# Kernel tuning notes

Hardware: AMD Instinct MI355X
Metric: run time of the kernel (lower is better)

The kernel has to match this reference:

```python
import jax, jax.numpy as jnp
import numpy as np

DIM = 256
H = W = 56
WS = 7           # window size
SHIFT = 3        # shift size
NH = 8           # num heads
HD = DIM // NH   # head dim
N = WS * WS      # tokens per window
SCALE = HD ** -0.5
EPS = 1e-5


def _rel_pos_index():
    coords = np.stack(np.meshgrid(np.arange(WS), np.arange(WS), indexing='ij'))  # (2,WS,WS)
    cf = coords.reshape(2, -1)                                # (2, N)
    rel = cf[:, :, None] - cf[:, None, :]                     # (2, N, N)
    rel = rel.transpose(1, 2, 0).astype(np.int64)             # (N, N, 2)
    rel[:, :, 0] += WS - 1
    rel[:, :, 1] += WS - 1
    rel[:, :, 0] *= 2 * WS - 1
    return rel.sum(-1)                                        # (N, N)

REL_IDX = _rel_pos_index()


def _attn_mask():
    # standard Swin shift mask: (nW, N, N) with 0 / -100
    img = np.zeros((H, W))
    cnt = 0
    for hs in (slice(0, -WS), slice(-WS, -SHIFT), slice(-SHIFT, None)):
        for ws in (slice(0, -WS), slice(-WS, -SHIFT), slice(-SHIFT, None)):
            img[hs, ws] = cnt
            cnt += 1
    win = img.reshape(H // WS, WS, W // WS, WS).transpose(0, 2, 1, 3).reshape(-1, N)  # (nW, N)
    diff = win[:, None, :] - win[:, :, None]
    return np.where(diff != 0, -100.0, 0.0).astype(np.float32)

ATTN_MASK = jnp.asarray(_attn_mask())  # (nW, N, N)


def _ln(x, g, b):
    mu = jnp.mean(x, -1, keepdims=True)
    var = jnp.mean(jnp.square(x - mu), -1, keepdims=True)
    return (x - mu) * jax.lax.rsqrt(var + EPS) * g + b


def _win_part(x):
    # (B,H,W,C) -> (B*nW, N, C)
    B, _, _, C = x.shape
    x = x.reshape(B, H // WS, WS, W // WS, WS, C)
    return x.transpose(0, 1, 3, 2, 4, 5).reshape(-1, N, C)


def _win_rev(xw, B):
    # (B*nW, N, C) -> (B,H,W,C)
    C = xw.shape[-1]
    x = xw.reshape(B, H // WS, W // WS, WS, WS, C)
    return x.transpose(0, 1, 3, 2, 4, 5).reshape(B, H, W, C)


def setup_inputs() -> dict:
    key = jax.random.key(0)
    ks = jax.random.split(key, 6)
    return {
        'x': jax.random.normal(ks[0], (32, H * W, DIM), jnp.float32),
        'norm1_g': jnp.ones((DIM,), jnp.float32),
        'norm1_b': jnp.zeros((DIM,), jnp.float32),
        'qkv_w': jax.random.normal(ks[1], (3 * DIM, DIM), jnp.float32) * 0.02,
        'qkv_b': jnp.zeros((3 * DIM,), jnp.float32),
        'rel_table': jax.random.normal(ks[2], ((2 * WS - 1) ** 2, NH), jnp.float32) * 0.02,
        'proj_w': jax.random.normal(ks[3], (DIM, DIM), jnp.float32) * 0.02,
        'proj_b': jnp.zeros((DIM,), jnp.float32),
        'norm2_g': jnp.ones((DIM,), jnp.float32),
        'norm2_b': jnp.zeros((DIM,), jnp.float32),
        'fc1_w': jax.random.normal(ks[4], (4 * DIM, DIM), jnp.float32) * 0.02,
        'fc1_b': jnp.zeros((4 * DIM,), jnp.float32),
        'fc2_w': jax.random.normal(ks[5], (DIM, 4 * DIM), jnp.float32) * 0.02,
        'fc2_b': jnp.zeros((DIM,), jnp.float32),
    }


def reference(x, norm1_g, norm1_b, qkv_w, qkv_b, rel_table, proj_w, proj_b,
              norm2_g, norm2_b, fc1_w, fc1_b, fc2_w, fc2_b):
    B = x.shape[0]
    shortcut = x
    h = _ln(x, norm1_g, norm1_b).reshape(B, H, W, DIM)
    # cyclic shift
    h = jnp.roll(h, (-SHIFT, -SHIFT), axis=(1, 2))
    xw = _win_part(h)                                  # (B*nW, N, C)
    Bw = xw.shape[0]
    qkv = (xw @ qkv_w.T + qkv_b).reshape(Bw, N, 3, NH, HD).transpose(2, 0, 3, 1, 4)
    q, k, v = qkv[0] * SCALE, qkv[1], qkv[2]           # (Bw, NH, N, HD)
    attn = jnp.einsum('bhnd,bhmd->bhnm', q, k)         # (Bw, NH, N, N)
    bias = rel_table[REL_IDX.reshape(-1)].reshape(N, N, NH).transpose(2, 0, 1)
    attn = attn + bias[None]
    nW = ATTN_MASK.shape[0]
    attn = attn.reshape(B, nW, NH, N, N) + ATTN_MASK[None, :, None]
    attn = jax.nn.softmax(attn.reshape(Bw, NH, N, N), axis=-1)
    out = jnp.einsum('bhnm,bhmd->bhnd', attn, v).transpose(0, 2, 1, 3).reshape(Bw, N, DIM)
    out = out @ proj_w.T + proj_b
    h = _win_rev(out, B)
    h = jnp.roll(h, (SHIFT, SHIFT), axis=(1, 2)).reshape(B, H * W, DIM)
    x = shortcut + h
    y = _ln(x, norm2_g, norm2_b)
    y = jax.nn.gelu(y @ fc1_w.T + fc1_b, approximate=False)
    y = y @ fc2_w.T + fc2_b
    return x + y
```

## Files before the change

### kernel.cpp

```cpp
#include <hip/hip_runtime.h>


typedef float f4 __attribute__((ext_vector_type(4)));
typedef __bf16 b8 __attribute__((ext_vector_type(8)));

#define DEV static __device__ __forceinline__

DEV ushort f2bf(float f) {
  union { __bf16 b; ushort u; } c; c.b = (__bf16)f;
  return c.u;
}
DEV __bf16 bfb(ushort u) { union { ushort u; __bf16 b; } c; c.u = u; return c.b; }
DEV b8 zero_b8() {
  b8 z;
#pragma unroll
  for (int i = 0; i < 8; ++i) z[i] = (__bf16)0.f;
  return z;
}
DEV void load_lds16(const void* g, void* l) {
  __builtin_amdgcn_global_load_lds(
      (const __attribute__((address_space(1))) unsigned int*)g,
      (__attribute__((address_space(3))) unsigned int*)l, 16, 0, 0);
}
DEV int reg3(int t) { return t < 49 ? 0 : (t < 53 ? 1 : 2); }

__global__ __launch_bounds__(256) void cast_w(const float* a, ushort* oa, int na,
                                              const float* b, ushort* ob, int nb,
                                              const float* c, ushort* oc, int nc,
                                              const float* d, ushort* od, int nd) {
  int total = na + nb + nc + nd;
  for (int i = blockIdx.x * 256 + threadIdx.x; i < total; i += gridDim.x * 256) {
    int j = i;
    if (j < na) { oa[j] = f2bf(a[j]); continue; }
    j -= na;
    if (j < nb) { ob[j] = f2bf(b[j]); continue; }
    j -= nb;
    if (j < nc) { oc[j] = f2bf(c[j]); continue; }
    j -= nc;
    od[j] = f2bf(d[j]);
  }
}

__global__ __launch_bounds__(256) void build_bias(const float* __restrict__ rel_table,
                                                  float* __restrict__ comb) {
  const int idx = blockIdx.x * 256 + threadIdx.x;
  if (idx >= 4 * 8 * 64 * 64) return;
  const int j = idx & 63, i = (idx >> 6) & 63, h = (idx >> 12) & 7, ty = idx >> 15;
  float v;
  if (i < 49 && j < 49) {
    const int iy = i / 7, ix = i - iy * 7, jy = j / 7, jx = j - jy * 7;
    const int ridx = (iy - jy + 6) * 13 + (ix - jx + 6);
    v = rel_table[ridx * 8 + h];
    const int wh = (ty & 2) ? 7 : 0, ww = (ty & 1) ? 7 : 0;
    const int irg = reg3(wh * 7 + iy) * 3 + reg3(ww * 7 + ix);
    const int jrg = reg3(wh * 7 + jy) * 3 + reg3(ww * 7 + jx);
    if (irg != jrg) v -= 100.f;
  } else {
    v = -1e30f;
  }
  comb[idx] = v;
}

__global__ __launch_bounds__(256) void ln_shift(const float* __restrict__ x,
                                                const float* __restrict__ g,
                                                const float* __restrict__ bta,
                                                ushort* __restrict__ out, int shifted) {
  const int wid = threadIdx.x >> 6, lane = threadIdx.x & 63;
  const int t = blockIdx.x * 4 + wid;
  int src;
  if (shifted) {
    int win = t / 49, n = t - win * 49;
    int bb = win >> 6, wh = (win >> 3) & 7, ww = win & 7;
    int wy = n / 7, wx = n - wy * 7;
    int r = wh * 7 + wy + 3; if (r >= 56) r -= 56;
    int c = ww * 7 + wx + 3; if (c >= 56) c -= 56;
    src = bb * 3136 + r * 56 + c;
  } else {
    src = t;
  }
  const float4 v = *(const float4*)(x + (size_t)src * 256 + lane * 4);
  float s  = v.x + v.y + v.z + v.w;
  float s2 = v.x * v.x + v.y * v.y + v.z * v.z + v.w * v.w;
#pragma unroll
  for (int m = 32; m; m >>= 1) { s += __shfl_xor(s, m); s2 += __shfl_xor(s2, m); }
  const float mean = s * (1.f / 256.f);
  const float var  = s2 * (1.f / 256.f) - mean * mean;
  const float rs   = rsqrtf(var + 1e-5f);
  const float4 gv = *(const float4*)(g + lane * 4);
  const float4 bv = *(const float4*)(bta + lane * 4);
  ushort4 o;
  o.x = f2bf((v.x - mean) * rs * gv.x + bv.x);
  o.y = f2bf((v.y - mean) * rs * gv.y + bv.y);
  o.z = f2bf((v.z - mean) * rs * gv.z + bv.z);
  o.w = f2bf((v.w - mean) * rs * gv.w + bv.w);
  *(ushort4*)(out + (size_t)t * 256 + lane * 4) = o;
}

template <class Epi>
__global__ __launch_bounds__(256, 4) void gemm_bt(const ushort* __restrict__ A,
                                                  const ushort* __restrict__ B,
                                                  int K, int NT, Epi epi) {
  __shared__ ushort lsA[2][128 * 32];
  __shared__ ushort lsB[2][128 * 32];
  const int tid = threadIdx.x;
  const int lane = tid & 63, wid = tid >> 6;
  const int quad = lane >> 4, l16 = lane & 15;
  const int wm = wid >> 1, wn = wid & 1;
  const int lin = blockIdx.x;
  const int xcd = lin & 7, j = lin >> 3;
  const int mt = xcd * 98 + j / NT;
  const int nt_ = j % NT;
  const long rowA0 = (long)mt * 128;
  const long colB0 = (long)nt_ * 128;
  f4 acc[4][4];
#pragma unroll
  for (int i = 0; i < 4; ++i)
#pragma unroll
    for (int jj = 0; jj < 4; ++jj) { acc[i][jj][0] = 0.f; acc[i][jj][1] = 0.f; acc[i][jj][2] = 0.f; acc[i][jj][3] = 0.f; }
  const int lrow = lane >> 2;
  const int lk = ((lane & 3) ^ ((lane >> 3) & 3)) * 8;
  const int rsw = (quad ^ ((l16 >> 1) & 3)) * 8;
  const int seg0 = wid * 2, seg1 = wid * 2 + 1;
  const ushort* pa0 = A + (rowA0 + seg0 * 16 + lrow) * (long)K + lk;
  const ushort* pa1 = A + (rowA0 + seg1 * 16 + lrow) * (long)K + lk;
  const ushort* pb0 = B + (colB0 + seg0 * 16 + lrow) * (long)K + lk;
  const ushort* pb1 = B + (colB0 + seg1 * 16 + lrow) * (long)K + lk;

  const int nsteps = K >> 5;
  load_lds16(pa0, &lsA[0][seg0 * 512]);
  load_lds16(pa1, &lsA[0][seg1 * 512]);
  load_lds16(pb0, &lsB[0][seg0 * 512]);
  load_lds16(pb1, &lsB[0][seg1 * 512]);
  __syncthreads();

  for (int t = 0; t < nsteps; ++t) {
    const int cur = t & 1;
    if (t + 1 < nsteps) {
      const int k1 = (t + 1) << 5;
      load_lds16(pa0 + k1, &lsA[cur ^ 1][seg0 * 512]);
      load_lds16(pa1 + k1, &lsA[cur ^ 1][seg1 * 512]);
      load_lds16(pb0 + k1, &lsB[cur ^ 1][seg0 * 512]);
      load_lds16(pb1 + k1, &lsB[cur ^ 1][seg1 * 512]);
    }
    b8 af[4], bfr[4];
#pragma unroll
    for (int ti = 0; ti < 4; ++ti)
      af[ti] = *(const b8*)&lsA[cur][(wm * 64 + ti * 16 + l16) * 32 + rsw];
#pragma unroll
    for (int tj = 0; tj < 4; ++tj)
      bfr[tj] = *(const b8*)&lsB[cur][(wn * 64 + tj * 16 + l16) * 32 + rsw];
#pragma unroll
    for (int ti = 0; ti < 4; ++ti)
#pragma unroll
      for (int tj = 0; tj < 4; ++tj)
        acc[ti][tj] = __builtin_amdgcn_mfma_f32_16x16x32_bf16(af[ti], bfr[tj], acc[ti][tj], 0, 0, 0);
    __syncthreads();
  }
#pragma unroll
  for (int ti = 0; ti < 4; ++ti)
#pragma unroll
    for (int tj = 0; tj < 4; ++tj)
#pragma unroll
      for (int r = 0; r < 4; ++r)
        epi((int)(rowA0 + wm * 64 + ti * 16 + quad * 4 + r),
            (int)(colB0 + wn * 64 + tj * 16 + l16), acc[ti][tj][r]);
}

struct QkvEpi {
  ushort* out; const float* bias;
  __device__ void operator()(int r, int c, float v) const {
    v += bias[c];
    if (c < 256) v *= 0.17677669529663687f;
    out[(size_t)r * 768 + c] = f2bf(v);
  }
};
struct GeluEpi {
  ushort* out; const float* bias;
  __device__ void operator()(int r, int c, float v) const {
    v += bias[c];
    v = 0.5f * v * (1.f + erff(v * 0.70710678118654752f));
    out[(size_t)r * 1024 + c] = f2bf(v);
  }
};
struct Fc2Epi {
  float* out; const float* bias;
  __device__ void operator()(int r, int c, float v) const {
    size_t i = (size_t)r * 256 + c;
    out[i] = out[i] + v + bias[c];
  }
};

__global__ __launch_bounds__(512) void attn_proj(const ushort* __restrict__ qkv,
                                                 const float* __restrict__ comb,
                                                 const ushort* __restrict__ projw,
                                                 const float* __restrict__ projb,
                                                 const float* __restrict__ x_in,
                                                 const float* __restrict__ n2g,
                                                 const float* __restrict__ n2b,
                                                 float* __restrict__ x_out,
                                                 ushort* __restrict__ xw2) {
  __shared__ ushort sbuf[32768];
  const int win = blockIdx.x;
  const int b = win >> 6, wh = (win >> 3) & 7, ww = win & 7;
  const int tid = threadIdx.x, lane = tid & 63, h = tid >> 6;
  const int quad = lane >> 4, l16 = lane & 15;
  const size_t wbase = (size_t)win * 49 * 768;

  b8 af[4], bfr[4];
#pragma unroll
  for (int ti = 0; ti < 4; ++ti) {
    const int tok = ti * 16 + l16;
    af[ti] = (tok < 49) ? *(const b8*)(qkv + wbase + (size_t)tok * 768 + h * 32 + quad * 8)
                        : zero_b8();
  }
#pragma unroll
  for (int tj = 0; tj < 4; ++tj) {
    const int key = tj * 16 + l16;
    bfr[tj] = (key < 49) ? *(const b8*)(qkv + wbase + (size_t)key * 768 + 256 + h * 32 + quad * 8)
                         : zero_b8();
  }
  f4 S[4][4];
#pragma unroll
  for (int ti = 0; ti < 4; ++ti)
#pragma unroll
    for (int tj = 0; tj < 4; ++tj) {
      S[ti][tj][0] = 0.f; S[ti][tj][1] = 0.f; S[ti][tj][2] = 0.f; S[ti][tj][3] = 0.f;
      S[ti][tj] = __builtin_amdgcn_mfma_f32_16x16x32_bf16(af[ti], bfr[tj], S[ti][tj], 0, 0, 0);
    }

  ushort* P = sbuf + h * 4096;
  const float* cmb = comb + ((((wh == 7) ? 2 : 0) + ((ww == 7) ? 1 : 0)) * 8 + h) * 4096;
#pragma unroll
  for (int ti = 0; ti < 4; ++ti) {
#pragma unroll
    for (int r = 0; r < 4; ++r) {
      const int i = ti * 16 + quad * 4 + r;
      const float* crow = cmb + i * 64 + l16;
      float sv[4];
#pragma unroll
      for (int tj = 0; tj < 4; ++tj) sv[tj] = S[ti][tj][r] + crow[tj * 16];
      float m = fmaxf(fmaxf(sv[0], sv[1]), fmaxf(sv[2], sv[3]));
#pragma unroll
      for (int d = 1; d < 16; d <<= 1) m = fmaxf(m, __shfl_xor(m, d));
      float sum = 0.f;
#pragma unroll
      for (int tj = 0; tj < 4; ++tj) { sv[tj] = __expf(sv[tj] - m); sum += sv[tj]; }
#pragma unroll
      for (int d = 1; d < 16; d <<= 1) sum += __shfl_xor(sum, d);
      const float inv = 1.f / sum;
      const int swz = i & 7, off = l16 & 7, cb = l16 >> 3;
#pragma unroll
      for (int tj = 0; tj < 4; ++tj) {
        const int cc = tj * 2 + cb;
        P[i * 64 + (((cc ^ swz) << 3) | off)] = f2bf(sv[tj] * inv);
      }
    }
  }

  f4 O[4][2];
#pragma unroll
  for (int ti = 0; ti < 4; ++ti)
#pragma unroll
    for (int tn = 0; tn < 2; ++tn) { O[ti][tn][0] = 0.f; O[ti][tn][1] = 0.f; O[ti][tn][2] = 0.f; O[ti][tn][3] = 0.f; }
#pragma unroll
  for (int kt = 0; kt < 2; ++kt) {
    b8 vb[2];
#pragma unroll
    for (int tn = 0; tn < 2; ++tn)
#pragma unroll
      for (int j = 0; j < 8; ++j) {
        const int key = kt * 32 + quad * 8 + j;
        vb[tn][j] = (key < 49)
            ? bfb(qkv[wbase + (size_t)key * 768 + 512 + h * 32 + tn * 16 + l16])
            : (__bf16)0.f;
      }
#pragma unroll
    for (int ti = 0; ti < 4; ++ti) {
      const int row = ti * 16 + l16;
      const b8 pa = *(const b8*)(P + row * 64 + (((kt * 4 + quad) ^ (row & 7)) << 3));
#pragma unroll
      for (int tn = 0; tn < 2; ++tn)
        O[ti][tn] = __builtin_amdgcn_mfma_f32_16x16x32_bf16(pa, vb[tn], O[ti][tn], 0, 0, 0);
    }
  }

  __syncthreads();
  ushort* ob = sbuf;
#pragma unroll
  for (int ti = 0; ti < 4; ++ti)
#pragma unroll
    for (int tn = 0; tn < 2; ++tn)
#pragma unroll
      for (int r = 0; r < 4; ++r) {
        const int tok = ti * 16 + quad * 4 + r;
        const int cc = h * 4 + tn * 2 + (l16 >> 3);
        ob[tok * 256 + (((cc ^ (tok & 7)) << 3) | (l16 & 7))] = f2bf(O[ti][tn][r]);
      }
  __syncthreads();

  f4 C[4][2];
#pragma unroll
  for (int ti = 0; ti < 4; ++ti)
#pragma unroll
    for (int tn = 0; tn < 2; ++tn) { C[ti][tn][0] = 0.f; C[ti][tn][1] = 0.f; C[ti][tn][2] = 0.f; C[ti][tn][3] = 0.f; }
  for (int k0 = 0; k0 < 256; k0 += 32) {
    b8 bw[2];
#pragma unroll
    for (int tn = 0; tn < 2; ++tn)
      bw[tn] = *(const b8*)(projw + (size_t)(h * 32 + tn * 16 + l16) * 256 + k0 + quad * 8);
#pragma unroll
    for (int ti = 0; ti < 4; ++ti) {
      const int row = ti * 16 + l16;
      const b8 pa = *(const b8*)(ob + row * 256 + ((((k0 >> 3) + quad) ^ (row & 7)) << 3));
#pragma unroll
      for (int tn = 0; tn < 2; ++tn)
        C[ti][tn] = __builtin_amdgcn_mfma_f32_16x16x32_bf16(pa, bw[tn], C[ti][tn], 0, 0, 0);
    }
  }

  __syncthreads();
  float* fbuf = (float*)sbuf;
#pragma unroll
  for (int ti = 0; ti < 4; ++ti)
#pragma unroll
    for (int r = 0; r < 4; ++r) {
      const int tok = ti * 16 + quad * 4 + r;
      const int swz = tok & 7;
#pragma unroll
      for (int tn = 0; tn < 2; ++tn) {
        const int c4 = h * 8 + tn * 4 + (l16 >> 2);
        fbuf[tok * 256 + (((c4 ^ swz) << 2) | (l16 & 3))] = C[ti][tn][r];
      }
    }
  __syncthreads();

  for (int t = h; t < 49; t += 8) {
    const int wy = t / 7, wx = t - wy * 7;
    int rr = wh * 7 + wy + 3; if (rr >= 56) rr -= 56;
    int cc = ww * 7 + wx + 3; if (cc >= 56) cc -= 56;
    const size_t base = ((size_t)b * 3136 + rr * 56 + cc) * 256;
    float4 v = *(float4*)&fbuf[t * 256 + ((lane ^ (t & 7)) << 2)];
    const float4 pb = *(const float4*)(projb + lane * 4);
    const float4 xr = *(const float4*)(x_in + base + lane * 4);
    v.x += pb.x + xr.x; v.y += pb.y + xr.y; v.z += pb.z + xr.z; v.w += pb.w + xr.w;
    *(float4*)(x_out + base + lane * 4) = v;
    float s  = v.x + v.y + v.z + v.w;
    float s2 = v.x * v.x + v.y * v.y + v.z * v.z + v.w * v.w;
#pragma unroll
    for (int m = 32; m; m >>= 1) { s += __shfl_xor(s, m); s2 += __shfl_xor(s2, m); }
    const float mean = s * (1.f / 256.f);
    const float var  = s2 * (1.f / 256.f) - mean * mean;
    const float rs   = rsqrtf(var + 1e-5f);
    const float4 gv = *(const float4*)(n2g + lane * 4);
    const float4 bv = *(const float4*)(n2b + lane * 4);
    ushort4 o;
    o.x = f2bf((v.x - mean) * rs * gv.x + bv.x);
    o.y = f2bf((v.y - mean) * rs * gv.y + bv.y);
    o.z = f2bf((v.z - mean) * rs * gv.z + bv.z);
    o.w = f2bf((v.w - mean) * rs * gv.w + bv.w);
    *(ushort4*)(xw2 + base + lane * 4) = o;
  }
}

extern "C" void kernel_launch(void* const* d_in, const int* in_sizes, int n_in,
                              void* d_out, int out_size, void* d_ws, size_t ws_size,
                              hipStream_t stream) {
  const float* x     = (const float*)d_in[0];
  const float* n1g   = (const float*)d_in[1];
  const float* n1b   = (const float*)d_in[2];
  const float* qkvw  = (const float*)d_in[3];
  const float* qkvb  = (const float*)d_in[4];
  const float* relt  = (const float*)d_in[5];
  const float* projw = (const float*)d_in[6];
  const float* projb = (const float*)d_in[7];
  const float* n2g   = (const float*)d_in[8];
  const float* n2b   = (const float*)d_in[9];
  const float* fc1w  = (const float*)d_in[10];
  const float* fc1b  = (const float*)d_in[11];
  const float* fc2w  = (const float*)d_in[12];
  const float* fc2b  = (const float*)d_in[13];
  float* out = (float*)d_out;
  char* ws = (char*)d_ws;

  ushort* xw     = (ushort*)ws;
  ushort* qkv    = (ushort*)(ws + 51380224);
  ushort* hidden = qkv;
  float*  comb   = (float*)(ws + 205520896);
  ushort* wqkv   = (ushort*)(ws + 51380224 + 205520896);
  ushort* wproj  = wqkv + 196608;
  ushort* wfc1   = wproj + 65536;
  ushort* wfc2   = wfc1 + 262144;

  cast_w<<<768, 256, 0, stream>>>(qkvw, wqkv, 196608, projw, wproj, 65536,
                                  fc1w, wfc1, 262144, fc2w, wfc2, 262144);
  build_bias<<<512, 256, 0, stream>>>(relt, comb);
  ln_shift<<<25088, 256, 0, stream>>>(x, n1g, n1b, xw, 1);
  gemm_bt<<<4704, 256, 0, stream>>>(xw, wqkv, 256, 6, QkvEpi{qkv, qkvb});
  attn_proj<<<2048, 512, 0, stream>>>(qkv, comb, wproj, projb, x, n2g, n2b, out, xw);
  gemm_bt<<<6272, 256, 0, stream>>>(xw, wfc1, 256, 8, GeluEpi{hidden, fc1b});
  gemm_bt<<<1568, 256, 0, stream>>>(hidden, wfc2, 1024, 2, Fc2Epi{out, fc2b});
}
```

Before: 654.0 us.

## Fuse fc1+GELU and fc2 into one MLP kernel keeping hidden tile in LDS

Replaces the two separate MLP GEMM launches with a single kernel. Each 512-thread block computes a 64-row tile of fc1 with GELU, stores the bf16 hidden activations in 128KB of swizzled LDS, then runs fc2 from LDS and accumulates into the output. This removes the global write and re-read of the 1024-wide hidden tensor. In exchange, occupancy is limited by the large LDS allocation, and the weights are read straight from global memory without LDS staging, so every block re-reads them.

```diff
diff --git a/kernel.cpp b/kernel.cpp
--- a/kernel.cpp
+++ b/kernel.cpp
@@ -174,21 +174,102 @@
     out[(size_t)r * 768 + c] = f2bf(v);
   }
 };
-struct GeluEpi {
-  ushort* out; const float* bias;
-  __device__ void operator()(int r, int c, float v) const {
-    v += bias[c];
-    v = 0.5f * v * (1.f + erff(v * 0.70710678118654752f));
-    out[(size_t)r * 1024 + c] = f2bf(v);
-  }
-};
-struct Fc2Epi {
-  float* out; const float* bias;
-  __device__ void operator()(int r, int c, float v) const {
-    size_t i = (size_t)r * 256 + c;
-    out[i] = out[i] + v + bias[c];
-  }
-};
+
+__global__ __launch_bounds__(512, 2) void mlp2(const ushort* __restrict__ A,
+                                               const ushort* __restrict__ w1,
+                                               const float* __restrict__ b1,
+                                               const ushort* __restrict__ w2,
+                                               const float* __restrict__ b2,
+                                               float* __restrict__ out) {
+  extern __shared__ __align__(16) ushort ls[];
+  ushort* lsA = ls;
+  ushort* lsH = ls;
+  const int tid = threadIdx.x, lane = tid & 63, h = tid >> 6;
+  const int quad = lane >> 4, l16 = lane & 15;
+  const long r0 = (long)blockIdx.x * 64;
+  const int lrow = lane >> 2;
+  const int lk = ((lane & 3) ^ ((lane >> 3) & 3)) * 8;
+  const int rsw = (quad ^ ((l16 >> 1) & 3)) * 8;
+
+#pragma unroll
+  for (int seg = 0; seg < 4; ++seg)
+    load_lds16(A + (r0 + seg * 16 + lrow) * 256 + h * 32 + lk,
+               &lsA[h * 2048 + seg * 512]);
+  __syncthreads();
+
+  f4 a1[4][8];
+#pragma unroll
+  for (int ti = 0; ti < 4; ++ti)
+#pragma unroll
+    for (int tn = 0; tn < 8; ++tn) { a1[ti][tn][0] = 0.f; a1[ti][tn][1] = 0.f; a1[ti][tn][2] = 0.f; a1[ti][tn][3] = 0.f; }
+#pragma unroll
+  for (int kc = 0; kc < 8; ++kc) {
+    b8 bw[8];
+#pragma unroll
+    for (int tn = 0; tn < 8; ++tn)
+      bw[tn] = *(const b8*)(w1 + (size_t)(h * 128 + tn * 16 + l16) * 256 + kc * 32 + quad * 8);
+    b8 af[4];
+#pragma unroll
+    for (int ti = 0; ti < 4; ++ti)
+      af[ti] = *(const b8*)&lsA[kc * 2048 + (ti * 16 + l16) * 32 + rsw];
+#pragma unroll
+    for (int ti = 0; ti < 4; ++ti)
+#pragma unroll
+      for (int tn = 0; tn < 8; ++tn)
+        a1[ti][tn] = __builtin_amdgcn_mfma_f32_16x16x32_bf16(af[ti], bw[tn], a1[ti][tn], 0, 0, 0);
+  }
+  __syncthreads();
+
+  float b1v[8];
+#pragma unroll
+  for (int tn = 0; tn < 8; ++tn) b1v[tn] = b1[h * 128 + tn * 16 + l16];
+#pragma unroll
+  for (int ti = 0; ti < 4; ++ti)
+#pragma unroll
+    for (int tn = 0; tn < 8; ++tn)
+#pragma unroll
+      for (int rr = 0; rr < 4; ++rr) {
+        const int row = ti * 16 + quad * 4 + rr;
+        const int cc = h * 16 + tn * 2 + (l16 >> 3);
+        float v = a1[ti][tn][rr] + b1v[tn];
+        v = 0.5f * v * (1.f + erff(v * 0.70710678118654752f));
+        lsH[row * 1024 + (((cc ^ (row & 7)) << 3) | (l16 & 7))] = f2bf(v);
+      }
+  __syncthreads();
+
+  f4 a2[4][2];
+#pragma unroll
+  for (int ti = 0; ti < 4; ++ti)
+#pragma unroll
+    for (int tn = 0; tn < 2; ++tn) { a2[ti][tn][0] = 0.f; a2[ti][tn][1] = 0.f; a2[ti][tn][2] = 0.f; a2[ti][tn][3] = 0.f; }
+#pragma unroll 8
+  for (int k0 = 0; k0 < 1024; k0 += 32) {
+    b8 bw2[2];
+#pragma unroll
+    for (int tn = 0; tn < 2; ++tn)
+      bw2[tn] = *(const b8*)(w2 + (size_t)(h * 32 + tn * 16 + l16) * 1024 + k0 + quad * 8);
+#pragma unroll
+    for (int ti = 0; ti < 4; ++ti) {
+      const int row = ti * 16 + l16;
+      const b8 pa = *(const b8*)&lsH[row * 1024 + ((((k0 >> 3) + quad) ^ (row & 7)) << 3)];
+#pragma unroll
+      for (int tn = 0; tn < 2; ++tn)
+        a2[ti][tn] = __builtin_amdgcn_mfma_f32_16x16x32_bf16(pa, bw2[tn], a2[ti][tn], 0, 0, 0);
+    }
+  }
+
+#pragma unroll
+  for (int tn = 0; tn < 2; ++tn) {
+    const float bb = b2[h * 32 + tn * 16 + l16];
+#pragma unroll
+    for (int ti = 0; ti < 4; ++ti)
+#pragma unroll
+      for (int rr = 0; rr < 4; ++rr) {
+        const size_t i = (size_t)(r0 + ti * 16 + quad * 4 + rr) * 256 + h * 32 + tn * 16 + l16;
+        out[i] += a2[ti][tn][rr] + bb;
+      }
+  }
+}
 
 __global__ __launch_bounds__(512) void attn_proj(const ushort* __restrict__ qkv,
                                                  const float* __restrict__ comb,
@@ -384,12 +465,18 @@
 
   ushort* xw     = (ushort*)ws;
   ushort* qkv    = (ushort*)(ws + 51380224);
-  ushort* hidden = qkv;
   float*  comb   = (float*)(ws + 205520896);
   ushort* wqkv   = (ushort*)(ws + 51380224 + 205520896);
   ushort* wproj  = wqkv + 196608;
   ushort* wfc1   = wproj + 65536;
   ushort* wfc2   = wfc1 + 262144;
+
+  static bool attr_done = false;
+  if (!attr_done) {
+    attr_done = true;
+    hipFuncSetAttribute(reinterpret_cast<const void*>(&mlp2),
+                        hipFuncAttributeMaxDynamicSharedMemorySize, 131072);
+  }
 
   cast_w<<<768, 256, 0, stream>>>(qkvw, wqkv, 196608, projw, wproj, 65536,
                                   fc1w, wfc1, 262144, fc2w, wfc2, 262144);
@@ -397,6 +484,5 @@
   ln_shift<<<25088, 256, 0, stream>>>(x, n1g, n1b, xw, 1);
   gemm_bt<<<4704, 256, 0, stream>>>(xw, wqkv, 256, 6, QkvEpi{qkv, qkvb});
   attn_proj<<<2048, 512, 0, stream>>>(qkv, comb, wproj, projb, x, n2g, n2b, out, xw);
-  gemm_bt<<<6272, 256, 0, stream>>>(xw, wfc1, 256, 8, GeluEpi{hidden, fc1b});
-  gemm_bt<<<1568, 256, 0, stream>>>(hidden, wfc2, 1024, 2, Fc2Epi{out, fc2b});
-}
+  mlp2<<<1568, 512, 131072, stream>>>(xw, wfc1, fc1b, wfc2, fc2b, out);
+}
```

Measured after the change: 698.1 us. +6.7%, slower.
